# Performance work log

Hardware: AMD Instinct MI355X
Metric: run time of the kernel (lower is better)

## Reference

```python
import jax, jax.numpy as jnp
import numpy as np

T = 8           # hardcoded frame count in forward
MAX_D = 3       # hardcoded displacement radius -> 7x7 = 49-entry cost volume
PATCH = 2 * MAX_D + 1
EPS = 1e-12     # F.normalize eps


def _l2norm_c(x):
    # x: [B, C, H, W]; L2-normalize over channel dim (torch F.normalize dim=1)
    n = jnp.sqrt(jnp.sum(x * x, axis=1, keepdims=True))
    return x / jnp.maximum(n, EPS)


def setup_inputs() -> dict:
    key = jax.random.key(0)
    ks = jax.random.split(key, 6)
    B, N, C = 2, 8192, 512
    nh = 8
    d = C // nh
    return {
        "x": jax.random.normal(ks[0], (B, N, C), jnp.float32),
        "w_qk": jax.random.normal(ks[1], (2 * C, C), jnp.float32) * 0.02,
        "w_corr": jax.random.normal(ks[2], (d, PATCH * PATCH), jnp.float32) * 0.02,
        "b_corr": jax.random.normal(ks[3], (d,), jnp.float32) * 0.02,
        "w_proj": jax.random.normal(ks[4], (C, C), jnp.float32) * 0.02,
        "b_proj": jax.random.normal(ks[5], (C,), jnp.float32) * 0.02,
    }


def reference(x, w_qk, w_corr, b_corr, w_proj, b_proj):
    B, N, C = x.shape
    nh = 8
    d = C // nh
    H = int(round((N // T) ** 0.5))
    W = H

    # qk projection (no bias): [B, N, 2C] -> [2, B, nh, N, d]
    qk = jnp.einsum('bnc,ec->bne', x, w_qk).reshape(B, N, 2, nh, d)
    q = jnp.transpose(qk[:, :, 0], (0, 2, 1, 3))  # [B, nh, N, d]
    k = jnp.transpose(qk[:, :, 1], (0, 2, 1, 3))

    # 'b n (t h w) d -> (b n) t d h w'
    def to_vid(a):
        a = a.reshape(B, nh, T, H, W, d)
        return jnp.transpose(a, (0, 1, 2, 5, 3, 4)).reshape(B * nh, T, d, H, W)

    q = to_vid(q)
    k = to_vid(k)

    # k_postfix: shift time forward, repeat last frame
    k_post = jnp.concatenate([k[:, 1:], k[:, -1:]], axis=1)

    BT = B * nh * T
    qf = _l2norm_c(q.reshape(BT, d, H, W))
    kf = _l2norm_c(k_post.reshape(BT, d, H, W))

    # local cost volume: corr[b, u*7+v, y, x] = sum_c qf[b,c,y,x] * kf[b,c,y+u-3,x+v-3]
    kp = jnp.pad(kf, ((0, 0), (0, 0), (MAX_D, MAX_D), (MAX_D, MAX_D)))
    corr = jnp.stack(
        [jnp.sum(qf * kp[:, :, u:u + H, v:v + W], axis=1)
         for u in range(PATCH) for v in range(PATCH)],
        axis=1,
    )  # [BT, 49, H, W]

    # 'b u v h w -> b (h w) (u v)'
    corr = jnp.transpose(corr, (0, 2, 3, 1)).reshape(BT, H * W, PATCH * PATCH)

    # proj_corr: 49 -> head_dim
    mf = jnp.einsum('bpk,dk->bpd', corr, w_corr) + b_corr  # [BT, HW, d]

    # '(b n t) (h w) d -> b (t h w) (n d)'
    mf = mf.reshape(B, nh, T, H, W, d)
    mf = jnp.transpose(mf, (0, 2, 3, 4, 1, 5)).reshape(B, N, C)

    # final projection
    return jnp.einsum('bnc,oc->bno', mf, w_proj) + b_proj
```

## Files before the change

### kernel.cpp

```cpp
#include <hip/hip_runtime.h>

typedef unsigned int u32;
typedef unsigned short u16;
typedef __fp16 h2 __attribute__((ext_vector_type(2)));
typedef __fp16 f16x8 __attribute__((ext_vector_type(8)));
typedef float f32x4 __attribute__((ext_vector_type(4)));

#define DEVFN static __device__ __forceinline__

DEVFN u32 pkh(float a, float b) {
  return __builtin_bit_cast(u32, __builtin_amdgcn_cvt_pkrtz(a, b));
}
DEVFN u16 f2h(float f) { __fp16 h = (__fp16)f; return __builtin_bit_cast(u16, h); }

#if __has_builtin(__builtin_amdgcn_fdot2)
DEVFN float dot2u(u32 a, u32 b, float c) {
  return __builtin_amdgcn_fdot2(__builtin_bit_cast(h2, a),
                                __builtin_bit_cast(h2, b), c, false);
}
#else
DEVFN float dot2u(u32 a, u32 b, float c) {
  h2 x = __builtin_bit_cast(h2, a), y = __builtin_bit_cast(h2, b);
  return c + (float)x[0] * (float)y[0] + (float)x[1] * (float)y[1];
}
#endif

DEVFN uint4 pk8(f32x4 lo, f32x4 hi) {
  uint4 o;
  o.x = pkh(lo.x, lo.y); o.y = pkh(lo.z, lo.w);
  o.z = pkh(hi.x, hi.y); o.w = pkh(hi.z, hi.w);
  return o;
}

DEVFN void gld16(const u16* g, u16* l) {
  __builtin_amdgcn_global_load_lds(
      (const __attribute__((address_space(1))) u32*)g,
      (__attribute__((address_space(3))) u32*)l, 16, 0, 0);
}

DEVFN void waitl0() { asm volatile("s_waitcnt lgkmcnt(0)" ::: "memory"); }
DEVFN void rbar() {
  __builtin_amdgcn_sched_barrier(0);
  __builtin_amdgcn_s_barrier();
  __builtin_amdgcn_sched_barrier(0);
}

template <int MODE, int F32, int TN>
__global__ __launch_bounds__(256) void gemm(
    const void* __restrict__ A_, const void* __restrict__ B_,
    const float* __restrict__ bias, void* __restrict__ Out_,
    int Nn, int K) {
  __shared__ u16 As[2][4096];
  __shared__ u16 Bs[2][4096];
  const int tid = threadIdx.x;
  const int lane = tid & 63;
  const int w = tid >> 6;
  const int wm = w >> 1, wn = w & 1;
  const int nwg = (int)gridDim.x;
  const int wg = ((int)blockIdx.x & 7) * (nwg >> 3) + ((int)blockIdx.x >> 3);
  const int tm = wg / TN, tn = wg % TN;

  const float* Af = (const float*)A_;
  const float* Bf = (const float*)B_;
  const u16* Ah = (const u16*)A_;
  const u16* Bh = (const u16*)B_;

  const int rr = tid >> 2;
  const int s8 = (tid & 3) << 3;
  const size_t offA = (size_t)(tm * 128 + rr) * K + s8;
  const size_t offB = (size_t)(tn * 128 + rr) * K + s8;
  const int wofs = rr * 32 + s8;

  const int sr = w * 32 + (lane >> 2);
  const int sc = (lane & 3) << 3;
  const u16* gA = Ah + (size_t)(tm * 128 + sr) * K + sc;
  const u16* gB = Bh + (size_t)(tn * 128 + sr) * K + sc;

  const int rofsA = ((wm * 64 + (lane & 15)) << 5) + ((lane >> 4) << 3);
  const int rofsB = ((wn * 64 + (lane & 15)) << 5) + ((lane >> 4) << 3);

  f32x4 acc[4][4] = {};

  f32x4 a0, a1, a2, a3, b0, b1, b2, b3;

#define LOADF(t)                                                          \
  {                                                                       \
    const size_t oa = offA + (size_t)(t) * 32;                            \
    const size_t ob = offB + (size_t)(t) * 32;                            \
    a0 = *(const f32x4*)(Af + oa);                                        \
    a1 = *(const f32x4*)(Af + oa + 4);                                    \
    a2 = *(const f32x4*)(Af + oa + (size_t)64 * K);                       \
    a3 = *(const f32x4*)(Af + oa + (size_t)64 * K + 4);                   \
    b0 = *(const f32x4*)(Bf + ob);                                        \
    b1 = *(const f32x4*)(Bf + ob + 4);                                    \
    b2 = *(const f32x4*)(Bf + ob + (size_t)64 * K);                       \
    b3 = *(const f32x4*)(Bf + ob + (size_t)64 * K + 4);                   \
  }
#define WRITEF(bufi)                                                      \
  {                                                                       \
    u16* da = &As[bufi][wofs];                                            \
    u16* db = &Bs[bufi][wofs];                                            \
    *(uint4*)da = pk8(a0, a1);                                            \
    *(uint4*)(da + 2048) = pk8(a2, a3);                                   \
    *(uint4*)db = pk8(b0, b1);                                            \
    *(uint4*)(db + 2048) = pk8(b2, b3);                                   \
  }
#define STAGEH(bufi, t)                                                   \
  {                                                                       \
    gld16(gA + (size_t)(t) * 32, &As[bufi][w * 1024]);                    \
    gld16(gA + (size_t)(t) * 32 + (size_t)16 * K, &As[bufi][w * 1024 + 512]); \
    gld16(gB + (size_t)(t) * 32, &Bs[bufi][w * 1024]);                    \
    gld16(gB + (size_t)(t) * 32 + (size_t)16 * K, &Bs[bufi][w * 1024 + 512]); \
  }

  if (F32) {
    const int KT = K >> 5;
    LOADF(0)
    WRITEF(0)
    LOADF(1)
    waitl0();
    rbar();
    for (int kt = 0; kt < KT; ++kt) {
      const int cur = kt & 1;
      f16x8 af[4], bf[4];
#pragma unroll
      for (int i = 0; i < 4; ++i) af[i] = *(const f16x8*)(&As[cur][rofsA + i * 512]);
#pragma unroll
      for (int i = 0; i < 4; ++i) bf[i] = *(const f16x8*)(&Bs[cur][rofsB + i * 512]);
      if (kt + 1 < KT) {
        WRITEF(cur ^ 1)
        if (kt + 2 < KT) LOADF(kt + 2)
      }
      __builtin_amdgcn_s_setprio(1);
#pragma unroll
      for (int mi = 0; mi < 4; ++mi)
#pragma unroll
        for (int ni = 0; ni < 4; ++ni)
          acc[mi][ni] = __builtin_amdgcn_mfma_f32_16x16x32_f16(af[mi], bf[ni],
                                                               acc[mi][ni], 0, 0, 0);
      __builtin_amdgcn_s_setprio(0);
      waitl0();
      rbar();
    }
  } else {
    const int KT = K >> 6;
    for (int kt = 0; kt < KT; ++kt) {
      __syncthreads();
      STAGEH(0, 2 * kt)
      STAGEH(1, 2 * kt + 1)
      __syncthreads();
#pragma unroll
      for (int sub = 0; sub < 2; ++sub) {
        f16x8 af[4], bf[4];
#pragma unroll
        for (int i = 0; i < 4; ++i)
          af[i] = *(const f16x8*)(&As[sub][rofsA + i * 512]);
#pragma unroll
        for (int i = 0; i < 4; ++i)
          bf[i] = *(const f16x8*)(&Bs[sub][rofsB + i * 512]);
#pragma unroll
        for (int mi = 0; mi < 4; ++mi)
#pragma unroll
          for (int ni = 0; ni < 4; ++ni)
            acc[mi][ni] = __builtin_amdgcn_mfma_f32_16x16x32_f16(
                af[mi], bf[ni], acc[mi][ni], 0, 0, 0);
      }
    }
  }
#undef LOADF
#undef WRITEF
#undef STAGEH

  const int rowBase = tm * 128 + wm * 64 + ((lane >> 4) << 2);
  const int colBase = tn * 128 + wn * 64 + (lane & 15);

  if (MODE == 1) {
    float* Out = (float*)Out_;
    float bv[4];
#pragma unroll
    for (int ni = 0; ni < 4; ++ni) bv[ni] = bias[colBase + ni * 16];
#pragma unroll
    for (int mi = 0; mi < 4; ++mi)
#pragma unroll
      for (int r = 0; r < 4; ++r) {
        size_t ro = (size_t)(rowBase + mi * 16 + r) * Nn;
#pragma unroll
        for (int ni = 0; ni < 4; ++ni)
          Out[ro + colBase + ni * 16] = acc[mi][ni][r] + bv[ni];
      }
  } else {
    u16* Out = (u16*)Out_;
    const int sel = colBase >> 9;
    const int hh = (colBase >> 6) & 7;
    const int ddb = lane & 15;
#pragma unroll
    for (int mi = 0; mi < 4; ++mi)
#pragma unroll
      for (int r = 0; r < 4; ++r) {
        float s = acc[mi][0][r] * acc[mi][0][r] + acc[mi][1][r] * acc[mi][1][r] +
                  acc[mi][2][r] * acc[mi][2][r] + acc[mi][3][r] * acc[mi][3][r];
        s += __shfl_xor(s, 1);
        s += __shfl_xor(s, 2);
        s += __shfl_xor(s, 4);
        s += __shfl_xor(s, 8);
        float inv = 1.0f / fmaxf(sqrtf(s), 1e-12f);
        const int m = rowBase + mi * 16 + r;
        const int bb = m >> 13, tt = (m >> 10) & 7, pix = m & 1023;
        const int fr = ((sel * 2 + bb) * 8 + tt) * 8 + hh;
        size_t base = (((size_t)fr) << 16) + (size_t)pix * 64 + ddb;
#pragma unroll
        for (int ni = 0; ni < 4; ++ni)
          Out[base + ni * 16] = f2h(acc[mi][ni][r] * inv);
      }
  }
}

__global__ __launch_bounds__(256) void dots_w2(
    const u16* __restrict__ qf, u16* __restrict__ corr,
    const float* __restrict__ wp, const float* __restrict__ wc,
    const float* __restrict__ bc, const float* __restrict__ bp,
    u16* __restrict__ W2, float* __restrict__ cvec) {
  __shared__ __align__(16) u16 smem[448 * 64];
  const int tid = threadIdx.x;

  if ((int)blockIdx.x >= 512) {
    const int o = (int)blockIdx.x - 512;
    float* wcl = (float*)smem;
    float* wpl = wcl + 3136;
    for (int i = tid; i < 3136; i += 256) wcl[i] = wc[i];
    wpl[tid] = wp[o * 512 + tid];
    wpl[tid + 256] = wp[o * 512 + tid + 256];
    __syncthreads();
#pragma unroll
    for (int pass = 0; pass < 2; ++pass) {
      const int idx = pass * 256 + tid;
      const int hh = idx >> 6, r = idx & 63, du = r >> 3, dv = r & 7;
      float sv = 0.f;
      if (du < 7 && dv < 7) {
#pragma unroll
        for (int c = 0; c < 64; ++c)
          sv += wpl[hh * 64 + c] * wcl[c * 49 + du * 7 + dv];
      }
      W2[o * 512 + idx] = f2h(sv);
    }
    if (tid < 64) {
      float p = 0.f;
#pragma unroll
      for (int g = 0; g < 8; ++g) p += wpl[g * 64 + tid];
      p *= bc[tid];
      p += __shfl_xor(p, 1); p += __shfl_xor(p, 2); p += __shfl_xor(p, 4);
      p += __shfl_xor(p, 8); p += __shfl_xor(p, 16); p += __shfl_xor(p, 32);
      if (tid == 0) cvec[o] = p + bp[o];
    }
    return;
  }

  u16* kst = smem;
  const int bid = ((int)blockIdx.x & 7) * 64 + ((int)blockIdx.x >> 3);
  const int fr = bid >> 2, grp = bid & 3;
  const int h = fr & 7, t = (fr >> 3) & 7, b = fr >> 6;
  const int t1 = (t < 7) ? t + 1 : 7;
  const int y0 = grp * 8;

  const u16* kbase = qf + (((size_t)(((2 + b) * 8 + t1) * 8 + h)) << 16);
  {
    const int ppx = tid >> 3;
    const int slot = tid & 7;
#pragma unroll
    for (int pass = 0; pass < 14; ++pass) {
      int gy = y0 - 3 + pass;
      uint4 v = make_uint4(0, 0, 0, 0);
      if ((unsigned)gy < 32u)
        v = *(const uint4*)(kbase + (size_t)(gy * 32 + ppx) * 64 + slot * 8);
      int pl = pass * 32 + ppx;
      *(uint4*)((char*)kst + pl * 128 + ((slot * 16) ^ ((pl & 7) << 4))) = v;
    }
  }

  const int px = grp * 256 + tid;
  const int x = tid & 31, yloc = tid >> 5;
  const u16* qp = qf + (((size_t)fr) << 16) + (size_t)px * 64;
  u32 qw[32];
#pragma unroll
  for (int j = 0; j < 8; ++j) {
    uint4 v = *(const uint4*)(qp + j * 8);
    qw[j * 4 + 0] = v.x; qw[j * 4 + 1] = v.y;
    qw[j * 4 + 2] = v.z; qw[j * 4 + 3] = v.w;
  }
  __syncthreads();

  u16* mp = corr + (size_t)((b * 8 + t) * 1024 + px) * 512 + h * 64;
  for (int du = 0; du < 7; ++du) {
    const int rlbase = (yloc + du) * 32;
    float f[7];
#pragma unroll
    for (int dv = 0; dv < 7; ++dv) {
      int xx = x + dv - 3;
      int xc = xx < 0 ? 0 : (xx > 31 ? 31 : xx);
      int pl = rlbase + xc;
      const char* kr = (const char*)kst + pl * 128;
      const int swz = (pl & 7) << 4;
      float s0 = 0.f, s1 = 0.f, s2 = 0.f, s3 = 0.f;
#pragma unroll
      for (int j = 0; j < 8; ++j) {
        uint4 v = *(const uint4*)(kr + ((j * 16) ^ swz));
        s0 = dot2u(qw[j * 4 + 0], v.x, s0);
        s1 = dot2u(qw[j * 4 + 1], v.y, s1);
        s2 = dot2u(qw[j * 4 + 2], v.z, s2);
        s3 = dot2u(qw[j * 4 + 3], v.w, s3);
      }
      float s = (s0 + s1) + (s2 + s3);
      f[dv] = ((unsigned)xx < 32u) ? s : 0.f;
    }
    uint4 o;
    o.x = pkh(f[0], f[1]); o.y = pkh(f[2], f[3]);
    o.z = pkh(f[4], f[5]); o.w = pkh(f[6], 0.f);
    *(uint4*)(mp + du * 8) = o;
  }
  *(uint4*)(mp + 56) = make_uint4(0, 0, 0, 0);
}

extern "C" void kernel_launch(void* const* d_in, const int* in_sizes, int n_in,
                              void* d_out, int out_size, void* d_ws, size_t ws_size,
                              hipStream_t stream) {
  const float* x      = (const float*)d_in[0];
  const float* w_qk   = (const float*)d_in[1];
  const float* w_corr = (const float*)d_in[2];
  const float* b_corr = (const float*)d_in[3];
  const float* w_proj = (const float*)d_in[4];
  const float* b_proj = (const float*)d_in[5];
  float* out = (float*)d_out;

  u16* corr = (u16*)d_ws;
  u16* qf   = corr + (size_t)16384 * 512;
  u16* W2   = qf + (size_t)16384 * 1024;
  float* cvec = (float*)(W2 + (size_t)512 * 512);

  gemm<0, 1, 8><<<dim3(1024), dim3(256), 0, stream>>>(
      x, w_qk, nullptr, qf, 1024, 512);
  dots_w2<<<dim3(1024), dim3(256), 0, stream>>>(qf, corr, w_proj, w_corr,
                                                b_corr, b_proj, W2, cvec);
  gemm<1, 0, 4><<<dim3(512), dim3(256), 0, stream>>>(
      corr, W2, cvec, out, 512, 512);
}
```

Measured before the change: 78.94 us.

## Compute two pixels per thread in cost volume and shrink padded K to 448

Each thread in the correlation kernel now handles two horizontally adjacent pixels, so every key row loaded from shared memory serves both pixels' dot products. This cuts LDS traffic from 14 to 8 key reads per du, and the block size is halved to 128 threads. The per-head cost-volume padding drops from 64 to 56 entries, giving a K dimension of 448 instead of 512 for the final GEMM and the W2 layout, which reduces GEMM work and intermediate bytes. The risks are higher register pressure from two q vectors and the kv buffer, fewer threads per block, and relying on the gemm template handling K=448 correctly.

```diff
diff --git a/kernel.cpp b/kernel.cpp
--- a/kernel.cpp
+++ b/kernel.cpp
@@ -215,7 +215,19 @@
   }
 }
 
-__global__ __launch_bounds__(256) void dots_w2(
+DEVFN float dot64(const u32* qw, const uint4* kv) {
+  float s0 = 0.f, s1 = 0.f, s2 = 0.f, s3 = 0.f;
+#pragma unroll
+  for (int j = 0; j < 8; ++j) {
+    s0 = dot2u(qw[j * 4 + 0], kv[j].x, s0);
+    s1 = dot2u(qw[j * 4 + 1], kv[j].y, s1);
+    s2 = dot2u(qw[j * 4 + 2], kv[j].z, s2);
+    s3 = dot2u(qw[j * 4 + 3], kv[j].w, s3);
+  }
+  return (s0 + s1) + (s2 + s3);
+}
+
+__global__ __launch_bounds__(128) void dots_w2(
     const u16* __restrict__ qf, u16* __restrict__ corr,
     const float* __restrict__ wp, const float* __restrict__ wc,
     const float* __restrict__ bc, const float* __restrict__ bp,
@@ -227,21 +239,22 @@
     const int o = (int)blockIdx.x - 512;
     float* wcl = (float*)smem;
     float* wpl = wcl + 3136;
-    for (int i = tid; i < 3136; i += 256) wcl[i] = wc[i];
-    wpl[tid] = wp[o * 512 + tid];
-    wpl[tid + 256] = wp[o * 512 + tid + 256];
+    for (int i = tid; i < 3136; i += 128) wcl[i] = wc[i];
+    for (int i = tid; i < 512; i += 128) wpl[i] = wp[o * 512 + i];
     __syncthreads();
 #pragma unroll
-    for (int pass = 0; pass < 2; ++pass) {
-      const int idx = pass * 256 + tid;
-      const int hh = idx >> 6, r = idx & 63, du = r >> 3, dv = r & 7;
-      float sv = 0.f;
-      if (du < 7 && dv < 7) {
-#pragma unroll
-        for (int c = 0; c < 64; ++c)
-          sv += wpl[hh * 64 + c] * wcl[c * 49 + du * 7 + dv];
-      }
-      W2[o * 512 + idx] = f2h(sv);
+    for (int pass = 0; pass < 4; ++pass) {
+      const int idx = pass * 128 + tid;
+      if (idx < 448) {
+        const int hh = idx / 56, r = idx % 56, du = r >> 3, dv = r & 7;
+        float sv = 0.f;
+        if (dv < 7) {
+#pragma unroll
+          for (int c = 0; c < 64; ++c)
+            sv += wpl[hh * 64 + c] * wcl[c * 49 + du * 7 + dv];
+        }
+        W2[o * 448 + idx] = f2h(sv);
+      }
     }
     if (tid < 64) {
       float p = 0.f;
@@ -267,57 +280,71 @@
     const int ppx = tid >> 3;
     const int slot = tid & 7;
 #pragma unroll
-    for (int pass = 0; pass < 14; ++pass) {
-      int gy = y0 - 3 + pass;
+    for (int pass = 0; pass < 28; ++pass) {
+      int pl = pass * 16 + ppx;
+      int gy = y0 - 3 + (pl >> 5);
+      int gx = pl & 31;
       uint4 v = make_uint4(0, 0, 0, 0);
       if ((unsigned)gy < 32u)
-        v = *(const uint4*)(kbase + (size_t)(gy * 32 + ppx) * 64 + slot * 8);
-      int pl = pass * 32 + ppx;
+        v = *(const uint4*)(kbase + (size_t)(gy * 32 + gx) * 64 + slot * 8);
       *(uint4*)((char*)kst + pl * 128 + ((slot * 16) ^ ((pl & 7) << 4))) = v;
     }
   }
 
-  const int px = grp * 256 + tid;
-  const int x = tid & 31, yloc = tid >> 5;
-  const u16* qp = qf + (((size_t)fr) << 16) + (size_t)px * 64;
-  u32 qw[32];
+  const int xh = tid & 15, yloc = tid >> 4;
+  const int px0 = grp * 256 + yloc * 32 + 2 * xh;
+  const int x0 = 2 * xh;
+  const u16* qp = qf + (((size_t)fr) << 16) + (size_t)px0 * 64;
+  u32 qw0[32], qw1[32];
 #pragma unroll
   for (int j = 0; j < 8; ++j) {
     uint4 v = *(const uint4*)(qp + j * 8);
-    qw[j * 4 + 0] = v.x; qw[j * 4 + 1] = v.y;
-    qw[j * 4 + 2] = v.z; qw[j * 4 + 3] = v.w;
+    qw0[j * 4 + 0] = v.x; qw0[j * 4 + 1] = v.y;
+    qw0[j * 4 + 2] = v.z; qw0[j * 4 + 3] = v.w;
+  }
+#pragma unroll
+  for (int j = 0; j < 8; ++j) {
+    uint4 v = *(const uint4*)(qp + 64 + j * 8);
+    qw1[j * 4 + 0] = v.x; qw1[j * 4 + 1] = v.y;
+    qw1[j * 4 + 2] = v.z; qw1[j * 4 + 3] = v.w;
   }
   __syncthreads();
 
-  u16* mp = corr + (size_t)((b * 8 + t) * 1024 + px) * 512 + h * 64;
+  const size_t tok0 = (size_t)((b * 8 + t) * 1024 + px0);
+  u16* mp0 = corr + tok0 * 448 + h * 56;
+  u16* mp1 = mp0 + 448;
+
   for (int du = 0; du < 7; ++du) {
-    const int rlbase = (yloc + du) * 32;
-    float f[7];
-#pragma unroll
-    for (int dv = 0; dv < 7; ++dv) {
-      int xx = x + dv - 3;
-      int xc = xx < 0 ? 0 : (xx > 31 ? 31 : xx);
-      int pl = rlbase + xc;
+    const int rlb = (yloc + du) * 32;
+    float f0[7], f1[7];
+#pragma unroll
+    for (int ci = 0; ci < 8; ++ci) {
+      int col = x0 + ci - 3;
+      unsigned inb = ((unsigned)col < 32u);
+      int xc = col < 0 ? 0 : (col > 31 ? 31 : col);
+      int pl = rlb + xc;
       const char* kr = (const char*)kst + pl * 128;
       const int swz = (pl & 7) << 4;
-      float s0 = 0.f, s1 = 0.f, s2 = 0.f, s3 = 0.f;
-#pragma unroll
-      for (int j = 0; j < 8; ++j) {
-        uint4 v = *(const uint4*)(kr + ((j * 16) ^ swz));
-        s0 = dot2u(qw[j * 4 + 0], v.x, s0);
-        s1 = dot2u(qw[j * 4 + 1], v.y, s1);
-        s2 = dot2u(qw[j * 4 + 2], v.z, s2);
-        s3 = dot2u(qw[j * 4 + 3], v.w, s3);
-      }
-      float s = (s0 + s1) + (s2 + s3);
-      f[dv] = ((unsigned)xx < 32u) ? s : 0.f;
-    }
-    uint4 o;
-    o.x = pkh(f[0], f[1]); o.y = pkh(f[2], f[3]);
-    o.z = pkh(f[4], f[5]); o.w = pkh(f[6], 0.f);
-    *(uint4*)(mp + du * 8) = o;
-  }
-  *(uint4*)(mp + 56) = make_uint4(0, 0, 0, 0);
+      uint4 kv[8];
+#pragma unroll
+      for (int j = 0; j < 8; ++j) kv[j] = *(const uint4*)(kr + ((j * 16) ^ swz));
+      if (ci < 7) {
+        float s = dot64(qw0, kv);
+        f0[ci] = inb ? s : 0.f;
+      }
+      if (ci > 0) {
+        float s = dot64(qw1, kv);
+        f1[ci - 1] = inb ? s : 0.f;
+      }
+    }
+    uint4 o0, o1;
+    o0.x = pkh(f0[0], f0[1]); o0.y = pkh(f0[2], f0[3]);
+    o0.z = pkh(f0[4], f0[5]); o0.w = pkh(f0[6], 0.f);
+    o1.x = pkh(f1[0], f1[1]); o1.y = pkh(f1[2], f1[3]);
+    o1.z = pkh(f1[4], f1[5]); o1.w = pkh(f1[6], 0.f);
+    *(uint4*)(mp0 + du * 8) = o0;
+    *(uint4*)(mp1 + du * 8) = o1;
+  }
 }
 
 extern "C" void kernel_launch(void* const* d_in, const int* in_sizes, int n_in,
@@ -332,14 +359,14 @@
   float* out = (float*)d_out;
 
   u16* corr = (u16*)d_ws;
-  u16* qf   = corr + (size_t)16384 * 512;
+  u16* qf   = corr + (size_t)16384 * 448;
   u16* W2   = qf + (size_t)16384 * 1024;
-  float* cvec = (float*)(W2 + (size_t)512 * 512);
+  float* cvec = (float*)(W2 + (size_t)512 * 448);
 
   gemm<0, 1, 8><<<dim3(1024), dim3(256), 0, stream>>>(
       x, w_qk, nullptr, qf, 1024, 512);
-  dots_w2<<<dim3(1024), dim3(256), 0, stream>>>(qf, corr, w_proj, w_corr,
+  dots_w2<<<dim3(1024), dim3(128), 0, stream>>>(qf, corr, w_proj, w_corr,
                                                 b_corr, b_proj, W2, cvec);
   gemm<1, 0, 4><<<dim3(512), dim3(256), 0, stream>>>(
-      corr, W2, cvec, out, 512, 512);
-}
+      corr, W2, cvec, out, 512, 448);
+}
```

Result: slower. 83.25 us (+5.5%).

## Compact correlation buffer to 56 per head and retile the final GEMM

Applied to the files above, without the earlier changes.

The correlation intermediate is stored with 56 entries per head (7x8) instead of 64, which cuts the final GEMM's K from 512 to 448 and the corr write/read traffic by about an eighth. The fused W2 weight is packed to match, and the zero-padding store is dropped. The final GEMM becomes its own kernel with 64x128 tiles and 1024 blocks, up from 512 blocks, to improve occupancy and load balance. This split trades a larger tile's operand reuse for more parallelism.

```diff
diff --git a/kernel.cpp b/kernel.cpp
--- a/kernel.cpp
+++ b/kernel.cpp
@@ -45,11 +45,9 @@
   __builtin_amdgcn_sched_barrier(0);
 }
 
-template <int MODE, int F32, int TN>
-__global__ __launch_bounds__(256) void gemm(
-    const void* __restrict__ A_, const void* __restrict__ B_,
-    const float* __restrict__ bias, void* __restrict__ Out_,
-    int Nn, int K) {
+__global__ __launch_bounds__(256) void gemm1(
+    const float* __restrict__ Af, const float* __restrict__ Bf,
+    u16* __restrict__ Out, int Nn, int K) {
   __shared__ u16 As[2][4096];
   __shared__ u16 Bs[2][4096];
   const int tid = threadIdx.x;
@@ -58,12 +56,7 @@
   const int wm = w >> 1, wn = w & 1;
   const int nwg = (int)gridDim.x;
   const int wg = ((int)blockIdx.x & 7) * (nwg >> 3) + ((int)blockIdx.x >> 3);
-  const int tm = wg / TN, tn = wg % TN;
-
-  const float* Af = (const float*)A_;
-  const float* Bf = (const float*)B_;
-  const u16* Ah = (const u16*)A_;
-  const u16* Bh = (const u16*)B_;
+  const int tm = wg >> 3, tn = wg & 7;
 
   const int rr = tid >> 2;
   const int s8 = (tid & 3) << 3;
@@ -71,16 +64,10 @@
   const size_t offB = (size_t)(tn * 128 + rr) * K + s8;
   const int wofs = rr * 32 + s8;
 
-  const int sr = w * 32 + (lane >> 2);
-  const int sc = (lane & 3) << 3;
-  const u16* gA = Ah + (size_t)(tm * 128 + sr) * K + sc;
-  const u16* gB = Bh + (size_t)(tn * 128 + sr) * K + sc;
-
   const int rofsA = ((wm * 64 + (lane & 15)) << 5) + ((lane >> 4) << 3);
   const int rofsB = ((wn * 64 + (lane & 15)) << 5) + ((lane >> 4) << 3);
 
   f32x4 acc[4][4] = {};
-
   f32x4 a0, a1, a2, a3, b0, b1, b2, b3;
 
 #define LOADF(t)                                                          \
@@ -105,114 +92,133 @@
     *(uint4*)db = pk8(b0, b1);                                            \
     *(uint4*)(db + 2048) = pk8(b2, b3);                                   \
   }
-#define STAGEH(bufi, t)                                                   \
+
+  const int KT = K >> 5;
+  LOADF(0)
+  WRITEF(0)
+  LOADF(1)
+  waitl0();
+  rbar();
+  for (int kt = 0; kt < KT; ++kt) {
+    const int cur = kt & 1;
+    f16x8 af[4], bf[4];
+#pragma unroll
+    for (int i = 0; i < 4; ++i) af[i] = *(const f16x8*)(&As[cur][rofsA + i * 512]);
+#pragma unroll
+    for (int i = 0; i < 4; ++i) bf[i] = *(const f16x8*)(&Bs[cur][rofsB + i * 512]);
+    if (kt + 1 < KT) {
+      WRITEF(cur ^ 1)
+      if (kt + 2 < KT) LOADF(kt + 2)
+    }
+    __builtin_amdgcn_s_setprio(1);
+#pragma unroll
+    for (int mi = 0; mi < 4; ++mi)
+#pragma unroll
+      for (int ni = 0; ni < 4; ++ni)
+        acc[mi][ni] = __builtin_amdgcn_mfma_f32_16x16x32_f16(af[mi], bf[ni],
+                                                             acc[mi][ni], 0, 0, 0);
+    __builtin_amdgcn_s_setprio(0);
+    waitl0();
+    rbar();
+  }
+#undef LOADF
+#undef WRITEF
+
+  const int rowBase = tm * 128 + wm * 64 + ((lane >> 4) << 2);
+  const int colBase = tn * 128 + wn * 64 + (lane & 15);
+  const int sel = colBase >> 9;
+  const int hh = (colBase >> 6) & 7;
+  const int ddb = lane & 15;
+#pragma unroll
+  for (int mi = 0; mi < 4; ++mi)
+#pragma unroll
+    for (int r = 0; r < 4; ++r) {
+      float s = acc[mi][0][r] * acc[mi][0][r] + acc[mi][1][r] * acc[mi][1][r] +
+                acc[mi][2][r] * acc[mi][2][r] + acc[mi][3][r] * acc[mi][3][r];
+      s += __shfl_xor(s, 1);
+      s += __shfl_xor(s, 2);
+      s += __shfl_xor(s, 4);
+      s += __shfl_xor(s, 8);
+      float inv = 1.0f / fmaxf(sqrtf(s), 1e-12f);
+      const int m = rowBase + mi * 16 + r;
+      const int bb = m >> 13, tt = (m >> 10) & 7, pix = m & 1023;
+      const int fr = ((sel * 2 + bb) * 8 + tt) * 8 + hh;
+      size_t base = (((size_t)fr) << 16) + (size_t)pix * 64 + ddb;
+#pragma unroll
+      for (int ni = 0; ni < 4; ++ni)
+        Out[base + ni * 16] = f2h(acc[mi][ni][r] * inv);
+    }
+}
+
+__global__ __launch_bounds__(256) void gemm2b(
+    const u16* __restrict__ A, const u16* __restrict__ B,
+    const float* __restrict__ bias, float* __restrict__ Out,
+    int Nn, int K) {
+  __shared__ u16 As[2][2048];
+  __shared__ u16 Bs[2][4096];
+  const int tid = threadIdx.x;
+  const int lane = tid & 63;
+  const int w = tid >> 6;
+  const int nwg = (int)gridDim.x;
+  const int wg = ((int)blockIdx.x & 7) * (nwg >> 3) + ((int)blockIdx.x >> 3);
+  const int tm = wg >> 2, tn = wg & 3;
+
+  const u16* gA = A + (size_t)(tm * 64 + w * 16 + (lane >> 2)) * K +
+                  ((lane & 3) << 3);
+  const u16* gB = B + (size_t)(tn * 128 + w * 32 + (lane >> 2)) * K +
+                  ((lane & 3) << 3);
+
+  const int rofsA = ((lane & 15) << 5) + ((lane >> 4) << 3);
+  const int rofsB = w * 1024 + ((lane & 15) << 5) + ((lane >> 4) << 3);
+
+  f32x4 acc[4][2] = {};
+
+#define STG(bufi, t)                                                      \
   {                                                                       \
-    gld16(gA + (size_t)(t) * 32, &As[bufi][w * 1024]);                    \
-    gld16(gA + (size_t)(t) * 32 + (size_t)16 * K, &As[bufi][w * 1024 + 512]); \
+    gld16(gA + (size_t)(t) * 32, &As[bufi][w * 512]);                     \
     gld16(gB + (size_t)(t) * 32, &Bs[bufi][w * 1024]);                    \
     gld16(gB + (size_t)(t) * 32 + (size_t)16 * K, &Bs[bufi][w * 1024 + 512]); \
   }
 
-  if (F32) {
-    const int KT = K >> 5;
-    LOADF(0)
-    WRITEF(0)
-    LOADF(1)
-    waitl0();
-    rbar();
-    for (int kt = 0; kt < KT; ++kt) {
-      const int cur = kt & 1;
-      f16x8 af[4], bf[4];
-#pragma unroll
-      for (int i = 0; i < 4; ++i) af[i] = *(const f16x8*)(&As[cur][rofsA + i * 512]);
-#pragma unroll
-      for (int i = 0; i < 4; ++i) bf[i] = *(const f16x8*)(&Bs[cur][rofsB + i * 512]);
-      if (kt + 1 < KT) {
-        WRITEF(cur ^ 1)
-        if (kt + 2 < KT) LOADF(kt + 2)
-      }
-      __builtin_amdgcn_s_setprio(1);
+  const int KT = K >> 6;
+  for (int kt = 0; kt < KT; ++kt) {
+    __syncthreads();
+    STG(0, 2 * kt)
+    STG(1, 2 * kt + 1)
+    __syncthreads();
+#pragma unroll
+    for (int sub = 0; sub < 2; ++sub) {
+      f16x8 af[4], bf[2];
+#pragma unroll
+      for (int i = 0; i < 4; ++i)
+        af[i] = *(const f16x8*)(&As[sub][rofsA + i * 512]);
+#pragma unroll
+      for (int i = 0; i < 2; ++i)
+        bf[i] = *(const f16x8*)(&Bs[sub][rofsB + i * 512]);
 #pragma unroll
       for (int mi = 0; mi < 4; ++mi)
 #pragma unroll
-        for (int ni = 0; ni < 4; ++ni)
-          acc[mi][ni] = __builtin_amdgcn_mfma_f32_16x16x32_f16(af[mi], bf[ni],
-                                                               acc[mi][ni], 0, 0, 0);
-      __builtin_amdgcn_s_setprio(0);
-      waitl0();
-      rbar();
-    }
-  } else {
-    const int KT = K >> 6;
-    for (int kt = 0; kt < KT; ++kt) {
-      __syncthreads();
-      STAGEH(0, 2 * kt)
-      STAGEH(1, 2 * kt + 1)
-      __syncthreads();
-#pragma unroll
-      for (int sub = 0; sub < 2; ++sub) {
-        f16x8 af[4], bf[4];
-#pragma unroll
-        for (int i = 0; i < 4; ++i)
-          af[i] = *(const f16x8*)(&As[sub][rofsA + i * 512]);
-#pragma unroll
-        for (int i = 0; i < 4; ++i)
-          bf[i] = *(const f16x8*)(&Bs[sub][rofsB + i * 512]);
-#pragma unroll
-        for (int mi = 0; mi < 4; ++mi)
-#pragma unroll
-          for (int ni = 0; ni < 4; ++ni)
-            acc[mi][ni] = __builtin_amdgcn_mfma_f32_16x16x32_f16(
-                af[mi], bf[ni], acc[mi][ni], 0, 0, 0);
-      }
-    }
-  }
-#undef LOADF
-#undef WRITEF
-#undef STAGEH
-
-  const int rowBase = tm * 128 + wm * 64 + ((lane >> 4) << 2);
-  const int colBase = tn * 128 + wn * 64 + (lane & 15);
-
-  if (MODE == 1) {
-    float* Out = (float*)Out_;
-    float bv[4];
-#pragma unroll
-    for (int ni = 0; ni < 4; ++ni) bv[ni] = bias[colBase + ni * 16];
-#pragma unroll
-    for (int mi = 0; mi < 4; ++mi)
-#pragma unroll
-      for (int r = 0; r < 4; ++r) {
-        size_t ro = (size_t)(rowBase + mi * 16 + r) * Nn;
-#pragma unroll
-        for (int ni = 0; ni < 4; ++ni)
-          Out[ro + colBase + ni * 16] = acc[mi][ni][r] + bv[ni];
-      }
-  } else {
-    u16* Out = (u16*)Out_;
-    const int sel = colBase >> 9;
-    const int hh = (colBase >> 6) & 7;
-    const int ddb = lane & 15;
-#pragma unroll
-    for (int mi = 0; mi < 4; ++mi)
-#pragma unroll
-      for (int r = 0; r < 4; ++r) {
-        float s = acc[mi][0][r] * acc[mi][0][r] + acc[mi][1][r] * acc[mi][1][r] +
-                  acc[mi][2][r] * acc[mi][2][r] + acc[mi][3][r] * acc[mi][3][r];
-        s += __shfl_xor(s, 1);
-        s += __shfl_xor(s, 2);
-        s += __shfl_xor(s, 4);
-        s += __shfl_xor(s, 8);
-        float inv = 1.0f / fmaxf(sqrtf(s), 1e-12f);
-        const int m = rowBase + mi * 16 + r;
-        const int bb = m >> 13, tt = (m >> 10) & 7, pix = m & 1023;
-        const int fr = ((sel * 2 + bb) * 8 + tt) * 8 + hh;
-        size_t base = (((size_t)fr) << 16) + (size_t)pix * 64 + ddb;
-#pragma unroll
-        for (int ni = 0; ni < 4; ++ni)
-          Out[base + ni * 16] = f2h(acc[mi][ni][r] * inv);
-      }
-  }
+        for (int ni = 0; ni < 2; ++ni)
+          acc[mi][ni] = __builtin_amdgcn_mfma_f32_16x16x32_f16(
+              af[mi], bf[ni], acc[mi][ni], 0, 0, 0);
+    }
+  }
+#undef STG
+
+  const int rowBase = tm * 64 + ((lane >> 4) << 2);
+  const int colBase = tn * 128 + w * 32 + (lane & 15);
+  float bv[2];
+#pragma unroll
+  for (int ni = 0; ni < 2; ++ni) bv[ni] = bias[colBase + ni * 16];
+#pragma unroll
+  for (int mi = 0; mi < 4; ++mi)
+#pragma unroll
+    for (int r = 0; r < 4; ++r) {
+      size_t ro = (size_t)(rowBase + mi * 16 + r) * Nn;
+#pragma unroll
+      for (int ni = 0; ni < 2; ++ni)
+        Out[ro + colBase + ni * 16] = acc[mi][ni][r] + bv[ni];
+    }
 }
 
 __global__ __launch_bounds__(256) void dots_w2(
@@ -234,14 +240,16 @@
 #pragma unroll
     for (int pass = 0; pass < 2; ++pass) {
       const int idx = pass * 256 + tid;
-      const int hh = idx >> 6, r = idx & 63, du = r >> 3, dv = r & 7;
-      float sv = 0.f;
-      if (du < 7 && dv < 7) {
-#pragma unroll
-        for (int c = 0; c < 64; ++c)
-          sv += wpl[hh * 64 + c] * wcl[c * 49 + du * 7 + dv];
+      if (idx < 448) {
+        const int hh = idx / 56, r = idx % 56, du = r >> 3, dv = r & 7;
+        float sv = 0.f;
+        if (dv < 7) {
+#pragma unroll
+          for (int c = 0; c < 64; ++c)
+            sv += wpl[hh * 64 + c] * wcl[c * 49 + du * 7 + dv];
+        }
+        W2[o * 448 + idx] = f2h(sv);
       }
-      W2[o * 512 + idx] = f2h(sv);
     }
     if (tid < 64) {
       float p = 0.f;
@@ -289,7 +297,7 @@
   }
   __syncthreads();
 
-  u16* mp = corr + (size_t)((b * 8 + t) * 1024 + px) * 512 + h * 64;
+  u16* mp = corr + (size_t)((b * 8 + t) * 1024 + px) * 448 + h * 56;
   for (int du = 0; du < 7; ++du) {
     const int rlbase = (yloc + du) * 32;
     float f[7];
@@ -317,7 +325,6 @@
     o.z = pkh(f[4], f[5]); o.w = pkh(f[6], 0.f);
     *(uint4*)(mp + du * 8) = o;
   }
-  *(uint4*)(mp + 56) = make_uint4(0, 0, 0, 0);
 }
 
 extern "C" void kernel_launch(void* const* d_in, const int* in_sizes, int n_in,
@@ -332,14 +339,13 @@
   float* out = (float*)d_out;
 
   u16* corr = (u16*)d_ws;
-  u16* qf   = corr + (size_t)16384 * 512;
+  u16* qf   = corr + (size_t)16384 * 448;
   u16* W2   = qf + (size_t)16384 * 1024;
-  float* cvec = (float*)(W2 + (size_t)512 * 512);
-
-  gemm<0, 1, 8><<<dim3(1024), dim3(256), 0, stream>>>(
-      x, w_qk, nullptr, qf, 1024, 512);
+  float* cvec = (float*)(W2 + (size_t)512 * 448);
+
+  gemm1<<<dim3(1024), dim3(256), 0, stream>>>(x, w_qk, qf, 1024, 512);
   dots_w2<<<dim3(1024), dim3(256), 0, stream>>>(qf, corr, w_proj, w_corr,
                                                 b_corr, b_proj, W2, cvec);
-  gemm<1, 0, 4><<<dim3(512), dim3(256), 0, stream>>>(
-      corr, W2, cvec, out, 512, 512);
-}
+  gemm2b<<<dim3(1024), dim3(256), 0, stream>>>(corr, W2, b_proj ? cvec : cvec,
+                                               out, 512, 448);
+}
```

After: 78.16 us. About the same (-1.0%).
